# Performance work log

Measured on AMD Instinct MI355X. Metric: run time of the kernel, lower is better.

## Reference

```python
import jax, jax.numpy as jnp
import numpy as np

B, N, D = 4, 4096, 1024
H, HD = 16, 64            # num_heads, head_dim (dim // num_heads)
K_ANCHOR = 256
SCALE = 1.0 / np.sqrt(float(HD))


def setup_inputs() -> dict:
    key = jax.random.key(0)
    ks = jax.random.split(key, 12)
    init = lambda k, shape, fan_in: jax.random.normal(k, shape, jnp.float32) * (1.0 / np.sqrt(fan_in))
    return {
        "x": jax.random.normal(ks[0], (B, N, D), jnp.float32),
        "Wq": init(ks[1], (D, H * HD), D), "bq": jnp.zeros((H * HD,), jnp.float32),
        "Wk": init(ks[2], (D, H * HD), D), "bk": jnp.zeros((H * HD,), jnp.float32),
        "Wv": init(ks[3], (D, H * HD), D), "bv": jnp.zeros((H * HD,), jnp.float32),
        "Wqt": init(ks[4], (D, D), D),     "bqt": jnp.zeros((D,), jnp.float32),
        "Wo": init(ks[5], (H * HD, D), H * HD), "bo": jnp.zeros((D,), jnp.float32),
        "num_anchor_tokens": K_ANCHOR,
    }


def _split_heads(t):
    # [B, S, H*HD] -> [B, H, S, HD]
    b, s, _ = t.shape
    return t.reshape(b, s, H, HD).transpose(0, 2, 1, 3)


def reference(x, Wq, bq, Wk, bk, Wv, bv, Wqt, bqt, Wo, bo, num_anchor_tokens):
    K = num_anchor_tokens  # static python int
    anchors = x[:, :K]     # [B, K, D]
    queries = x[:, K:]     # [B, N-K, D]

    q_a = anchors @ Wq + bq           # [B, K, H*HD]
    k_a = anchors @ Wk + bk           # [B, K, H*HD]
    v_a = anchors @ Wv + bv           # [B, K, H*HD]
    q_q = queries @ Wqt + bqt         # [B, N-K, H*HD] (dim == H*HD)

    q = _split_heads(jnp.concatenate([q_a, q_q], axis=1))  # [B, H, N, HD]
    k = _split_heads(k_a)                                  # [B, H, K, HD]
    v = _split_heads(v_a)                                  # [B, H, K, HD]

    scores = jnp.einsum("bhnd,bhkd->bhnk", q, k) * SCALE   # [B, H, N, K]
    weights = jax.nn.softmax(scores, axis=-1)
    ctx = jnp.einsum("bhnk,bhkd->bhnd", weights, v)        # [B, H, N, HD]
    ctx = ctx.transpose(0, 2, 1, 3).reshape(x.shape[0], x.shape[1], H * HD)
    return ctx @ Wo + bo               # [B, N, D]
```

## Files before the change

kernel.cpp:

```cpp
#include <hip/hip_runtime.h>
#include <stdint.h>
#include <stddef.h>


typedef _Float16 v8hf __attribute__((ext_vector_type(8)));
typedef _Float16 h4   __attribute__((ext_vector_type(4)));
typedef float    f32x4 __attribute__((ext_vector_type(4)));
typedef uint32_t u32x4 __attribute__((ext_vector_type(4)));

#define ATT_SCALE 0.125f
#define LOG2E     1.44269504088896340736f
#define QK_CE     (ATT_SCALE * LOG2E)

__device__ __forceinline__ void async16(const void* g, void* l) {
  __builtin_amdgcn_global_load_lds(
      (const __attribute__((address_space(1))) void*)g,
      (__attribute__((address_space(3))) void*)l,
      16, 0, 0);
}

__device__ __forceinline__ uint32_t pk_h2(float a, float b) {
  auto w = __builtin_amdgcn_cvt_pkrtz(a, b);
  return __builtin_bit_cast(uint32_t, w);
}

__global__ __launch_bounds__(256) void cvt_kernel(const float* __restrict__ src,
                                                  _Float16* __restrict__ dst, int n) {
  int i = (blockIdx.x * 256 + threadIdx.x) * 4;
  if (i + 3 < n) {
    float4 v = *(const float4*)(src + i);
    h4 o; o[0] = (_Float16)v.x; o[1] = (_Float16)v.y; o[2] = (_Float16)v.z; o[3] = (_Float16)v.w;
    *(h4*)(dst + i) = o;
  }
}

struct TPArgs { const float* src[5]; _Float16* dst[5]; };

__global__ __launch_bounds__(256) void transpose5_k(TPArgs a) {
  __shared__ _Float16 t[32][33];
  const int z = blockIdx.z;
  const float* __restrict__ src = a.src[z];
  _Float16* __restrict__ dst = a.dst[z];
  const int bx = blockIdx.x * 32, by = blockIdx.y * 32;
  const int x = threadIdx.x;
  for (int yy = threadIdx.y; yy < 32; yy += 8)
    t[yy][x] = (_Float16)src[(size_t)(by + yy) * 1024 + bx + x];
  __syncthreads();
  for (int yy = threadIdx.y; yy < 32; yy += 8)
    dst[(size_t)(bx + yy) * 1024 + by + x] = t[x][yy];
}

template <typename OutT>
__global__ __launch_bounds__(512, 2) void gemm256(
    const _Float16* __restrict__ A, const _Float16* __restrict__ Bt,
    const float* __restrict__ bias, OutT* __restrict__ out,
    int rowsPerBatch, int rowStart, float oscale)
{
  __shared__ __attribute__((aligned(16))) _Float16 As[4 * 256 * 32];
  __shared__ __attribute__((aligned(16))) _Float16 Bs[4 * 256 * 32];

  const int tid  = threadIdx.x;
  const int wave = tid >> 6, lane = tid & 63;
  const int quad = lane >> 4, l16 = lane & 15;
  const int wr = wave >> 2, wc = wave & 3;

  const int nwg = gridDim.x * gridDim.y;
  const int lin = blockIdx.y * 4 + blockIdx.x;
  const int swz = (lin & 7) * (nwg >> 3) + (lin >> 3);
  const int bx = swz & 3, by = swz >> 2;

  const int lrow = lane >> 2, lblk = lane & 3;

  auto gRowOf = [&](int m) -> int {
    int b = m / rowsPerBatch;
    return b * 4096 + rowStart + (m - b * rowsPerBatch);
  };

  const int tr0 = wave * 16 + lrow;
  const int tr1 = 128 + tr0;
  const _Float16* aS0 = A  + (size_t)gRowOf(by * 256 + tr0) * 1024 + (lblk ^ ((tr0 >> 1) & 3)) * 8;
  const _Float16* aS1 = A  + (size_t)gRowOf(by * 256 + tr1) * 1024 + (lblk ^ ((tr1 >> 1) & 3)) * 8;
  const _Float16* bS0 = Bt + (size_t)(bx * 256 + tr0) * 1024 + (lblk ^ ((tr0 >> 1) & 3)) * 8;
  const _Float16* bS1 = Bt + (size_t)(bx * 256 + tr1) * 1024 + (lblk ^ ((tr1 >> 1) & 3)) * 8;

  auto stage = [&](int t) {
    const int k0 = t * 32;
    _Float16* ad = As + (t & 3) * 8192 + wave * 512;
    _Float16* bd = Bs + (t & 3) * 8192 + wave * 512;
    async16(aS0 + k0, ad);
    async16(aS1 + k0, ad + 4096);
    async16(bS0 + k0, bd);
    async16(bS1 + k0, bd + 4096);
  };

  const int fblk = (quad ^ ((l16 >> 1) & 3)) * 8;

  f32x4 acc[8][4];
  #pragma unroll
  for (int i = 0; i < 8; i++)
    #pragma unroll
    for (int j = 0; j < 4; j++)
      acc[i][j] = f32x4{0.f, 0.f, 0.f, 0.f};

  stage(0); stage(1); stage(2);

  #pragma unroll 1
  for (int t = 0; t < 32; ++t) {
    if (t < 30)       asm volatile("s_waitcnt vmcnt(8)" ::: "memory");
    else if (t == 30) asm volatile("s_waitcnt vmcnt(4)" ::: "memory");
    else              asm volatile("s_waitcnt vmcnt(0)" ::: "memory");
    __builtin_amdgcn_s_barrier();
    __builtin_amdgcn_sched_barrier(0);
    asm volatile("" ::: "memory");

    if (t + 3 < 32) stage(t + 3);

    const _Float16* Ab = As + (t & 3) * 8192;
    const _Float16* Bb = Bs + (t & 3) * 8192;
    v8hf af[8], bf[4];
    #pragma unroll
    for (int nt = 0; nt < 4; nt++)
      bf[nt] = *(const v8hf*)(Bb + (wc * 64 + nt * 16 + l16) * 32 + fblk);
    #pragma unroll
    for (int mt = 0; mt < 8; mt++)
      af[mt] = *(const v8hf*)(Ab + (wr * 128 + mt * 16 + l16) * 32 + fblk);

    __builtin_amdgcn_s_setprio(1);
    #pragma unroll
    for (int mt = 0; mt < 8; mt++)
      #pragma unroll
      for (int nt = 0; nt < 4; nt++)
        acc[mt][nt] = __builtin_amdgcn_mfma_f32_16x16x32_f16(af[mt], bf[nt], acc[mt][nt], 0, 0, 0);
    __builtin_amdgcn_s_setprio(0);
  }

  const int colBase = bx * 256 + wc * 64;
  const int rowBase = by * 256 + wr * 128;
  #pragma unroll
  for (int mt = 0; mt < 8; mt++) {
    #pragma unroll
    for (int r = 0; r < 4; r++) {
      int m = rowBase + mt * 16 + quad * 4 + r;
      int b = m / rowsPerBatch;
      int rr = m - b * rowsPerBatch;
      #pragma unroll
      for (int nt = 0; nt < 4; nt++) {
        int col = colBase + nt * 16 + l16;
        float v = (acc[mt][nt][r] + bias[col]) * oscale;
        out[(size_t)(b * 4096 + rowStart + rr) * 1024 + col] = (OutT)v;
      }
    }
  }
}

template <typename OutT>
__global__ __launch_bounds__(256) void gemm64(
    const _Float16* __restrict__ A, const _Float16* __restrict__ Bt,
    const float* __restrict__ bias0, const float* __restrict__ bias1,
    const float* __restrict__ bias2,
    OutT* __restrict__ out0, _Float16* __restrict__ out1, _Float16* __restrict__ out2,
    int rowsPerBatch, int rowStart, int mode)
{
  __shared__ __attribute__((aligned(16))) _Float16 As[64 * 32];
  __shared__ __attribute__((aligned(16))) _Float16 Bs[128 * 32];

  const int tid  = threadIdx.x;
  const int wave = tid >> 6, lane = tid & 63;
  const int quad = lane >> 4, l16 = lane & 15;
  const int wr = wave >> 1, wc = wave & 1;

  const int gx = gridDim.x;
  const int lin = blockIdx.y * gx + blockIdx.x;
  const int x8 = lin & 7, j = lin >> 3;
  const int bx = j % gx;
  const int by = x8 * (gridDim.y >> 3) + j / gx;

  const int srow = lane >> 2;
  const int skol = (((lane & 3) ^ ((lane >> 3) & 3)) * 8);

  auto gRowOf = [&](int m) -> int {
    int b = m / rowsPerBatch;
    int r = m - b * rowsPerBatch;
    return b * 4096 + rowStart + r;
  };

  const int bc0 = wave * 2, bc1 = bc0 + 1;
  const _Float16* aS  = A  + (size_t)gRowOf(by * 64 + wave * 16 + srow) * 1024 + skol;
  const _Float16* bS0 = Bt + (size_t)(bx * 128 + bc0 * 16 + srow) * 1024 + skol;
  const _Float16* bS1 = Bt + (size_t)(bx * 128 + bc1 * 16 + srow) * 1024 + skol;
  _Float16* aD  = As + wave * 512;
  _Float16* bD0 = Bs + bc0 * 512;
  _Float16* bD1 = Bs + bc1 * 512;

  const int fblk = (quad ^ ((l16 >> 1) & 3)) * 8;

  f32x4 acc[2][4];
  #pragma unroll
  for (int i = 0; i < 2; i++)
    #pragma unroll
    for (int jj = 0; jj < 4; jj++)
      acc[i][jj] = f32x4{0.f, 0.f, 0.f, 0.f};

  for (int k0 = 0; k0 < 1024; k0 += 32) {
    __syncthreads();
    async16(aS  + k0, aD);
    async16(bS0 + k0, bD0);
    async16(bS1 + k0, bD1);
    __syncthreads();

    v8hf af[2], bfr[4];
    #pragma unroll
    for (int mt = 0; mt < 2; mt++)
      af[mt] = *(const v8hf*)(As + (wr * 32 + mt * 16 + l16) * 32 + fblk);
    #pragma unroll
    for (int nt = 0; nt < 4; nt++)
      bfr[nt] = *(const v8hf*)(Bs + (wc * 64 + nt * 16 + l16) * 32 + fblk);
    #pragma unroll
    for (int mt = 0; mt < 2; mt++)
      #pragma unroll
      for (int nt = 0; nt < 4; nt++)
        acc[mt][nt] = __builtin_amdgcn_mfma_f32_16x16x32_f16(af[mt], bfr[nt], acc[mt][nt], 0, 0, 0);
  }

  const int colBase = bx * 128 + wc * 64;
  const int rowBase = by * 64 + wr * 32;
  #pragma unroll
  for (int mt = 0; mt < 2; mt++) {
    #pragma unroll
    for (int r = 0; r < 4; r++) {
      int m = rowBase + mt * 16 + quad * 4 + r;
      int b = m / rowsPerBatch;
      int rr = m - b * rowsPerBatch;
      #pragma unroll
      for (int nt = 0; nt < 4; nt++) {
        int col = colBase + nt * 16 + l16;
        float v = acc[mt][nt][r];
        if (mode == 0) {
          v += bias0[col];
          out0[(size_t)(b * 4096 + rowStart + rr) * 1024 + col] = (OutT)v;
        } else {
          if (col < 1024) {
            v = (v + bias0[col]) * QK_CE;
            out0[(size_t)(b * 4096 + rr) * 1024 + col] = (OutT)v;
          } else if (col < 2048) {
            int c2 = col - 1024;
            v += bias1[c2];
            out1[(size_t)(b * 256 + rr) * 1024 + c2] = (_Float16)v;
          } else {
            int c2 = col - 2048;
            v += bias2[c2];
            int pr = ((rr & 15) << 4) | (rr >> 4);
            out2[(size_t)((b * 16 + (c2 >> 6)) * 64 + (c2 & 63)) * 256 + pr] = (_Float16)v;
          }
        }
      }
    }
  }
}

__global__ __launch_bounds__(256) void attn_kernel(
    const _Float16* __restrict__ q, const _Float16* __restrict__ k,
    const _Float16* __restrict__ vt, _Float16* __restrict__ ctx)
{
  __shared__ __attribute__((aligned(16))) _Float16 KP[256 * 64];
  __shared__ __attribute__((aligned(16))) _Float16 Vs[64 * 256];

  const int tid  = threadIdx.x;
  const int wave = tid >> 6, lane = tid & 63;
  const int quad = lane >> 4, l16 = lane & 15;
  const int bid = blockIdx.x;
  const int qt = bid & 63, h = (bid >> 6) & 15, b = bid >> 10;

  const int fq = (l16 ^ (l16 >> 1)) & 7;

  const _Float16* kbase = k + (size_t)b * 256 * 1024 + h * 64;
  {
    const int s = lane >> 3;
    const int p = lane & 7;
    #pragma unroll
    for (int i = 0; i < 8; i++) {
      int c = wave * 8 + i;
      int row = c * 8 + s;
      int f = (row ^ (row >> 1)) & 7;
      async16(kbase + (size_t)row * 1024 + (p ^ f) * 8, KP + c * 512);
    }
  }

  const _Float16* vbase = vt + (size_t)(b * 16 + h) * 16384;
  {
    const int p = lane & 31;
    #pragma unroll
    for (int i = 0; i < 8; i++) {
      int c = wave * 8 + i;
      int d = c * 2 + (lane >> 5);
      int f = (d ^ (d >> 1)) & 7;
      async16(vbase + d * 256 + (p ^ f) * 8, Vs + c * 512);
    }
  }

  const int qrow = qt * 64 + wave * 16 + l16;
  const _Float16* qbase = q + (size_t)(b * 4096 + qrow) * 1024 + h * 64 + quad * 8;
  v8hf a0 = *(const v8hf*)(qbase);
  v8hf a1 = *(const v8hf*)(qbase + 32);

  f32x4 s[16];
  #pragma unroll
  for (int t = 0; t < 16; t++) s[t] = f32x4{0.f, 0.f, 0.f, 0.f};

  __syncthreads();

  #pragma unroll
  for (int t = 0; t < 16; t++) {
    const _Float16* rbase = KP + (t * 16 + l16) * 64;
    int pb0 = (quad ^ fq) * 8;
    v8hf b0 = *(const v8hf*)(rbase + pb0);
    v8hf b1 = *(const v8hf*)(rbase + (pb0 ^ 32));
    s[t] = __builtin_amdgcn_mfma_f32_16x16x32_f16(a0, b0, s[t], 0, 0, 0);
    s[t] = __builtin_amdgcn_mfma_f32_16x16x32_f16(a1, b1, s[t], 0, 0, 0);
  }

  float inv[4];
  #pragma unroll
  for (int r = 0; r < 4; r++) {
    float m01 = fmaxf(s[0][r], s[1][r]),   m23 = fmaxf(s[2][r], s[3][r]);
    float m45 = fmaxf(s[4][r], s[5][r]),   m67 = fmaxf(s[6][r], s[7][r]);
    float m89 = fmaxf(s[8][r], s[9][r]),   mab = fmaxf(s[10][r], s[11][r]);
    float mcd = fmaxf(s[12][r], s[13][r]), mef = fmaxf(s[14][r], s[15][r]);
    float m = fmaxf(fmaxf(fmaxf(m01, m23), fmaxf(m45, m67)),
                    fmaxf(fmaxf(m89, mab), fmaxf(mcd, mef)));
    m = fmaxf(m, __shfl_xor(m, 1));
    m = fmaxf(m, __shfl_xor(m, 2));
    m = fmaxf(m, __shfl_xor(m, 4));
    m = fmaxf(m, __shfl_xor(m, 8));
    float sum = 0.f;
    #pragma unroll
    for (int t = 0; t < 16; t++) {
      float e = exp2f(s[t][r] - m);
      s[t][r] = e;
      sum += e;
    }
    sum += __shfl_xor(sum, 1);
    sum += __shfl_xor(sum, 2);
    sum += __shfl_xor(sum, 4);
    sum += __shfl_xor(sum, 8);
    inv[r] = 1.0f / sum;
  }

  __syncthreads();

  #pragma unroll
  for (int r = 0; r < 4; r++) {
    const int qr = quad * 4 + r;
    const int fp = (qr ^ (qr >> 1)) & 7;
    _Float16* prow = KP + (wave * 16 + qr) * 256;
    u32x4 lo, hi;
    #pragma unroll
    for (int j = 0; j < 4; j++) {
      lo[j] = pk_h2(s[2 * j][r],     s[2 * j + 1][r]);
      hi[j] = pk_h2(s[2 * j + 8][r], s[2 * j + 9][r]);
    }
    *(u32x4*)(prow + ((2 * l16) ^ fp) * 8)     = lo;
    *(u32x4*)(prow + ((2 * l16 + 1) ^ fp) * 8) = hi;
  }

  asm volatile("s_waitcnt lgkmcnt(0)" ::: "memory");
  __builtin_amdgcn_sched_barrier(0);

  f32x4 o[4];
  #pragma unroll
  for (int nt = 0; nt < 4; nt++) o[nt] = f32x4{0.f, 0.f, 0.f, 0.f};
  #pragma unroll
  for (int c = 0; c < 8; c++) {
    int kblk = c * 4 + quad;
    v8hf pa = *(const v8hf*)(KP + (wave * 16 + l16) * 256 + (kblk ^ fq) * 8);
    #pragma unroll
    for (int nt = 0; nt < 4; nt++) {
      v8hf vb = *(const v8hf*)(Vs + (nt * 16 + l16) * 256 + (kblk ^ fq) * 8);
      o[nt] = __builtin_amdgcn_mfma_f32_16x16x32_f16(pa, vb, o[nt], 0, 0, 0);
    }
  }

  _Float16* obase = ctx + (size_t)(b * 4096 + qt * 64 + wave * 16 + quad * 4) * 1024 + h * 64;
  #pragma unroll
  for (int nt = 0; nt < 4; nt++)
    #pragma unroll
    for (int r = 0; r < 4; r++)
      obase[(size_t)r * 1024 + nt * 16 + l16] = (_Float16)(o[nt][r] * inv[r]);
}

extern "C" void kernel_launch(void* const* d_in, const int* in_sizes, int n_in,
                              void* d_out, int out_size, void* d_ws, size_t ws_size,
                              hipStream_t stream)
{
  (void)in_sizes; (void)n_in; (void)out_size; (void)ws_size;

  const float* x   = (const float*)d_in[0];
  const float* Wq  = (const float*)d_in[1];
  const float* bq  = (const float*)d_in[2];
  const float* Wk  = (const float*)d_in[3];
  const float* bk  = (const float*)d_in[4];
  const float* Wv  = (const float*)d_in[5];
  const float* bv  = (const float*)d_in[6];
  const float* Wqt = (const float*)d_in[7];
  const float* bqt = (const float*)d_in[8];
  const float* Wo  = (const float*)d_in[9];
  const float* bo  = (const float*)d_in[10];

  char* ws = (char*)d_ws;
  _Float16* xh    = (_Float16*)(ws);
  _Float16* WtQKV = (_Float16*)(ws + (32ll << 20));
  _Float16* WtQT  = (_Float16*)(ws + (38ll << 20));
  _Float16* WtO   = (_Float16*)(ws + (40ll << 20));
  _Float16* qbuf  = (_Float16*)(ws + (42ll << 20));
  _Float16* kbuf  = (_Float16*)(ws + (74ll << 20));
  _Float16* vtb   = (_Float16*)(ws + (76ll << 20));
  _Float16* ctxb  = (_Float16*)(ws + (78ll << 20));
  float* outp = (float*)d_out;

  const int nx = 4 * 4096 * 1024;
  cvt_kernel<<<nx / 1024, 256, 0, stream>>>(x, xh, nx);

  TPArgs tpa;
  tpa.src[0] = Wq;  tpa.dst[0] = WtQKV;
  tpa.src[1] = Wk;  tpa.dst[1] = WtQKV + 1024 * 1024;
  tpa.src[2] = Wv;  tpa.dst[2] = WtQKV + 2 * 1024 * 1024;
  tpa.src[3] = Wqt; tpa.dst[3] = WtQT;
  tpa.src[4] = Wo;  tpa.dst[4] = WtO;
  transpose5_k<<<dim3(32, 32, 5), dim3(32, 8), 0, stream>>>(tpa);

  gemm64<_Float16><<<dim3(24, 16), 256, 0, stream>>>(xh, WtQKV, bq, bk, bv,
                                                     qbuf, kbuf, vtb, 256, 0, 1);
  gemm256<_Float16><<<dim3(4, 60), 512, 0, stream>>>(xh, WtQT, bqt,
                                                     qbuf, 3840, 256, QK_CE);
  attn_kernel<<<4096, 256, 0, stream>>>(qbuf, kbuf, vtb, ctxb);
  gemm256<float><<<dim3(4, 64), 512, 0, stream>>>(ctxb, WtO, bo,
                                                  outp, 4096, 0, 1.0f);
}
```

Measured before the change: 324.7 us.

## Pre-swizzle V into MFMA fragment order and read it from global, dropping LDS staging

The projection epilogue now writes V in a layout that matches the MFMA B-fragment order, so each lane loads its 16-byte fragment straight from global memory (L2) during the PV matmul. This removes the V staging buffer in LDS. LDS use per block halves, and the launch bounds now request 5 blocks per CU to raise occupancy. P is stored with a permuted key order to match the new V ordering. The risk is that global or L2 latency on the V loads in the inner loop replaces fast LDS reads.

```diff
diff --git a/kernel.cpp b/kernel.cpp
--- a/kernel.cpp
+++ b/kernel.cpp
@@ -249,8 +249,11 @@
           } else {
             int c2 = col - 2048;
             v += bias2[c2];
-            int pr = ((rr & 15) << 4) | (rr >> 4);
-            out2[(size_t)((b * 16 + (c2 >> 6)) * 64 + (c2 & 63)) * 256 + pr] = (_Float16)v;
+            int hh = c2 >> 6, d = c2 & 63;
+            int kk = ((rr >> 7) & 1) * 128 + (rr & 15) * 8 + ((rr >> 4) & 7);
+            int idx = ((kk >> 5) * 4 + (d >> 4)) * 512
+                    + (((kk >> 3) & 3) * 16 + (d & 15)) * 8 + (kk & 7);
+            out2[(size_t)(b * 16 + hh) * 16384 + idx] = (_Float16)v;
           }
         }
       }
@@ -258,12 +261,11 @@
   }
 }
 
-__global__ __launch_bounds__(256) void attn_kernel(
+__global__ __launch_bounds__(256, 5) void attn_kernel(
     const _Float16* __restrict__ q, const _Float16* __restrict__ k,
     const _Float16* __restrict__ vt, _Float16* __restrict__ ctx)
 {
   __shared__ __attribute__((aligned(16))) _Float16 KP[256 * 64];
-  __shared__ __attribute__((aligned(16))) _Float16 Vs[64 * 256];
 
   const int tid  = threadIdx.x;
   const int wave = tid >> 6, lane = tid & 63;
@@ -283,18 +285,6 @@
       int row = c * 8 + s;
       int f = (row ^ (row >> 1)) & 7;
       async16(kbase + (size_t)row * 1024 + (p ^ f) * 8, KP + c * 512);
-    }
-  }
-
-  const _Float16* vbase = vt + (size_t)(b * 16 + h) * 16384;
-  {
-    const int p = lane & 31;
-    #pragma unroll
-    for (int i = 0; i < 8; i++) {
-      int c = wave * 8 + i;
-      int d = c * 2 + (lane >> 5);
-      int f = (d ^ (d >> 1)) & 7;
-      async16(vbase + d * 256 + (p ^ f) * 8, Vs + c * 512);
     }
   }
 
@@ -359,23 +349,23 @@
       lo[j] = pk_h2(s[2 * j][r],     s[2 * j + 1][r]);
       hi[j] = pk_h2(s[2 * j + 8][r], s[2 * j + 9][r]);
     }
-    *(u32x4*)(prow + ((2 * l16) ^ fp) * 8)     = lo;
-    *(u32x4*)(prow + ((2 * l16 + 1) ^ fp) * 8) = hi;
+    *(u32x4*)(prow + (l16 ^ fp) * 8)        = lo;
+    *(u32x4*)(prow + ((l16 ^ fp) + 16) * 8) = hi;
   }
 
   asm volatile("s_waitcnt lgkmcnt(0)" ::: "memory");
   __builtin_amdgcn_sched_barrier(0);
 
+  const _Float16* vlane = vt + (size_t)(b * 16 + h) * 16384 + lane * 8;
   f32x4 o[4];
   #pragma unroll
   for (int nt = 0; nt < 4; nt++) o[nt] = f32x4{0.f, 0.f, 0.f, 0.f};
   #pragma unroll
   for (int c = 0; c < 8; c++) {
-    int kblk = c * 4 + quad;
-    v8hf pa = *(const v8hf*)(KP + (wave * 16 + l16) * 256 + (kblk ^ fq) * 8);
+    v8hf pa = *(const v8hf*)(KP + (wave * 16 + l16) * 256 + ((c * 4 + quad) ^ fq) * 8);
     #pragma unroll
     for (int nt = 0; nt < 4; nt++) {
-      v8hf vb = *(const v8hf*)(Vs + (nt * 16 + l16) * 256 + (kblk ^ fq) * 8);
+      v8hf vb = *(const v8hf*)(vlane + (c * 4 + nt) * 512);
       o[nt] = __builtin_amdgcn_mfma_f32_16x16x32_f16(pa, vb, o[nt], 0, 0, 0);
     }
   }
```

Result: faster. 310.0 us (-4.5%).
